# Optimization experiments

Measured on AMD Instinct MI355X. Metric: run time of the kernel, lower is better.

## Reference

```python
import jax, jax.numpy as jnp
import numpy as np

DIM = 768
NUM_HEADS = 12
HEAD_DIM = DIM // NUM_HEADS
SCALE = HEAD_DIM ** -0.5


def setup_inputs() -> dict:
    key = jax.random.key(0)
    ks = jax.random.split(key, 7)
    B, N = 4, 2048
    s = DIM ** -0.5
    return {
        "x": jax.random.normal(ks[0], (B, N, DIM), dtype=jnp.float32),
        "attn_bias": jax.random.normal(ks[1], (1, NUM_HEADS, N, N), dtype=jnp.float32),
        "Wq": jax.random.normal(ks[2], (DIM, DIM), dtype=jnp.float32) * s,
        "Wk": jax.random.normal(ks[3], (DIM, DIM), dtype=jnp.float32) * s,
        "Wv": jax.random.normal(ks[4], (DIM, DIM), dtype=jnp.float32) * s,
        "Wp": jax.random.normal(ks[5], (DIM, DIM), dtype=jnp.float32) * s,
        "bp": jax.random.normal(ks[6], (DIM,), dtype=jnp.float32) * 0.02,
    }


def reference(x, attn_bias, Wq, Wk, Wv, Wp, bp):
    B, N, C = x.shape
    # Linear layers use y = x @ W.T (torch convention); split heads: [B,H,N,D]
    def heads(y):
        return y.reshape(B, N, NUM_HEADS, HEAD_DIM).transpose(0, 2, 1, 3)
    q = heads(x @ Wq.T)
    k = heads(x @ Wk.T)
    v = heads(x @ Wv.T)
    attn = jnp.einsum("bhnd,bhmd->bhnm", q, k) * SCALE + attn_bias
    attn = jax.nn.softmax(attn, axis=-1)
    out = jnp.einsum("bhnm,bhmd->bhnd", attn, v)
    out = out.transpose(0, 2, 1, 3).reshape(B, N, C)
    return out @ Wp.T + bp
```

## Files before the change

kernel.cpp:

```cpp
#include <hip/hip_runtime.h>
#include <hip/hip_bf16.h>

#define NTOK 2048
#define NHEADS 12
#define HDIM 64
#define DIM 768
#define BATCH 4
#define SC2_ 0.18033688011112042f

typedef __attribute__((ext_vector_type(8))) short short8;
typedef __attribute__((ext_vector_type(4))) float f32x4;
typedef __attribute__((ext_vector_type(16))) float f32x16;

__device__ __forceinline__ short f2bf(float f) {
  union { float f; unsigned u; } v; v.f = f;
  unsigned r = v.u + 0x7fffu + ((v.u >> 16) & 1u);
  return (short)(r >> 16);
}

__device__ __forceinline__ f32x4 mfma_bf16(short8 a, short8 b, f32x4 c) {
  return __builtin_amdgcn_mfma_f32_16x16x32_bf16(a, b, c, 0, 0, 0);
}

__device__ __forceinline__ f32x16 mfma32(short8 a, short8 b, f32x16 c) {
  return __builtin_amdgcn_mfma_f32_32x32x16_bf16(a, b, c, 0, 0, 0);
}

__device__ __forceinline__ void gload_lds16(const void* g, void* l) {
  __builtin_amdgcn_global_load_lds((const __attribute__((address_space(1))) void*)g,
                                   (__attribute__((address_space(3))) void*)l, 16, 0, 0);
}

__device__ __forceinline__ float exp2_hw(float x) {
  float r; asm("v_exp_f32 %0, %1" : "=v"(r) : "v"(x)); return r;
}

__device__ __forceinline__ unsigned cvt_pk_bf16(float lo, float hi) {
  unsigned r; asm("v_cvt_pk_bf16_f32 %0, %1, %2" : "=v"(r) : "v"(lo), "v"(hi)); return r;
}

__global__ void cvt_x(const float* __restrict__ src, short* __restrict__ dst) {
  int i = blockIdx.x * 256 + threadIdx.x;
  float4 v = ((const float4*)src)[i];
  short4 o; o.x = f2bf(v.x); o.y = f2bf(v.y); o.z = f2bf(v.z); o.w = f2bf(v.w);
  ((short4*)dst)[i] = o;
}

__global__ void cvt_w(const float* __restrict__ w0, const float* __restrict__ w1,
                      const float* __restrict__ w2, const float* __restrict__ w3,
                      short* __restrict__ d0, short* __restrict__ d1,
                      short* __restrict__ d2, short* __restrict__ d3) {
  int i = blockIdx.x * 256 + threadIdx.x;
  const float* s = blockIdx.y == 0 ? w0 : blockIdx.y == 1 ? w1 : blockIdx.y == 2 ? w2 : w3;
  short* d = blockIdx.y == 0 ? d0 : blockIdx.y == 1 ? d1 : blockIdx.y == 2 ? d2 : d3;
  float4 v = ((const float4*)s)[i];
  short4 o; o.x = f2bf(v.x); o.y = f2bf(v.y); o.z = f2bf(v.z); o.w = f2bf(v.w);
  ((short4*)d)[i] = o;
}

__device__ __forceinline__ void gemm_mainloop(const short* __restrict__ A,
                                              const short* __restrict__ B,
                                              int mbase, int nbase,
                                              short* As, short* Bs,
                                              f32x4 (&acc)[4][4], int lane, int w) {
  int lr = lane & 15, lg = lane >> 4;
  int wr = w >> 1, wc = w & 1;
  for (int kb = 0; kb < DIM; kb += 64) {
    if (kb) __syncthreads();
#pragma unroll
    for (int c = 0; c < 4; ++c) {
      int row = w * 32 + c * 8 + (lane >> 3);
      int sch = (lane & 7) ^ (row & 7);
      gload_lds16(A + (size_t)(mbase + row) * DIM + kb + sch * 8, (char*)As + w * 4096 + c * 1024);
      gload_lds16(B + (size_t)(nbase + row) * DIM + kb + sch * 8, (char*)Bs + w * 4096 + c * 1024);
    }
    __syncthreads();
#pragma unroll
    for (int ks = 0; ks < 2; ++ks) {
      short8 af[4], bf[4];
#pragma unroll
      for (int i = 0; i < 4; ++i) {
        int row = wr * 64 + i * 16 + lr;
        int ch = (ks * 4 + lg) ^ (row & 7);
        af[i] = *(const short8*)(As + row * 64 + ch * 8);
      }
#pragma unroll
      for (int j = 0; j < 4; ++j) {
        int row = wc * 64 + j * 16 + lr;
        int ch = (ks * 4 + lg) ^ (row & 7);
        bf[j] = *(const short8*)(Bs + row * 64 + ch * 8);
      }
#pragma unroll
      for (int i = 0; i < 4; ++i)
#pragma unroll
        for (int j = 0; j < 4; ++j)
          acc[i][j] = mfma_bf16(af[i], bf[j], acc[i][j]);
    }
  }
}

__global__ __launch_bounds__(256, 2) void gemm_qkv(const short* __restrict__ xb,
    const short* __restrict__ wq, const short* __restrict__ wk, const short* __restrict__ wv,
    short* __restrict__ Qh, short* __restrict__ Kh, short* __restrict__ Vt) {
  __shared__ __align__(16) short As[128 * 64];
  __shared__ __align__(16) short Bs[128 * 64];
  int nt = blockIdx.x, mt = blockIdx.y, z = blockIdx.z;
  const short* B = z == 0 ? wq : (z == 1 ? wk : wv);
  int tid = threadIdx.x, lane = tid & 63, w = tid >> 6;
  f32x4 acc[4][4] = {};
  gemm_mainloop(xb, B, mt * 128, nt * 128, As, Bs, acc, lane, w);
  int lr = lane & 15, lg = lane >> 4, wr = w >> 1, wc = w & 1;
  if (z < 2) {
    short* dst = z == 0 ? Qh : Kh;
#pragma unroll
    for (int i = 0; i < 4; ++i)
#pragma unroll
      for (int j = 0; j < 4; ++j) {
        int m = mt * 128 + wr * 64 + i * 16 + lg * 4;
        int n = nt * 128 + wc * 64 + j * 16 + lr;
        int bb = m >> 11, nn = m & 2047, hh = n >> 6, d = n & 63;
        size_t base = (((size_t)bb * NHEADS + hh) * NTOK + nn) * HDIM + d;
#pragma unroll
        for (int r = 0; r < 4; ++r)
          dst[base + (size_t)r * HDIM] = f2bf(acc[i][j][r]);
      }
  } else {
#pragma unroll
    for (int i = 0; i < 4; ++i)
#pragma unroll
      for (int j = 0; j < 4; ++j) {
        int m = mt * 128 + wr * 64 + i * 16 + lg * 4;
        int n = nt * 128 + wc * 64 + j * 16 + lr;
        int bb = m >> 11, nn = m & 2047, hh = n >> 6, d = n & 63;
        short4 pk;
        pk.x = f2bf(acc[i][j][0]); pk.y = f2bf(acc[i][j][1]);
        pk.z = f2bf(acc[i][j][2]); pk.w = f2bf(acc[i][j][3]);
        *(short4*)(Vt + (((size_t)bb * NHEADS + hh) * HDIM + d) * NTOK + nn) = pk;
      }
  }
}

__global__ __launch_bounds__(256, 3) void attn_fused(const short* __restrict__ Qh,
    const short* __restrict__ Kh, const short* __restrict__ Vt,
    const float* __restrict__ bias, short* __restrict__ Ob) {
  __shared__ __align__(16) short Ks[2][64 * 64];
  __shared__ __align__(16) short Vs[2][64 * 64];
  int d0 = blockIdx.x;
  int wg = (d0 & 7) * 96 + (d0 >> 3);
  int b = wg & 3, qb = (wg >> 2) & 15, h = wg >> 6;
  int tid = threadIdx.x, lane = tid & 63, w = tid >> 6;
  int ql = lane & 31, hi = lane >> 5, sx = ql & 7;

  const short* Q = Qh + ((size_t)b * NHEADS + h) * NTOK * HDIM;
  const short* K = Kh + ((size_t)b * NHEADS + h) * NTOK * HDIM;
  const short* V = Vt + ((size_t)b * NHEADS + h) * HDIM * NTOK;
  int qrow = qb * 128 + w * 32 + ql;
  const float* Bb = bias + ((size_t)h * NTOK + qrow) * NTOK;

  short8 qf[4];
#pragma unroll
  for (int i = 0; i < 4; ++i)
    qf[i] = *(const short8*)(Q + (size_t)qrow * HDIM + i * 16 + hi * 8);

  float psum = 0.f;
  f32x16 oacc[2] = {};

  auto stage = [&](int buf, int kv) {
#pragma unroll
    for (int c = 0; c < 2; ++c) {
      int row = w * 16 + c * 8 + (lane >> 3);
      int sch = (lane & 7) ^ (lane >> 3);
      gload_lds16(K + (size_t)(kv + row) * HDIM + sch * 8, (char*)Ks[buf] + w * 2048 + c * 1024);
      gload_lds16(V + (size_t)row * NTOK + kv + sch * 8, (char*)Vs[buf] + w * 2048 + c * 1024);
    }
  };

  stage(0, 0);
  __syncthreads();

  auto body = [&](int t, int cur) {
    int kv = t * 64;

    f32x16 sacc[2];
#pragma unroll
    for (int kb = 0; kb < 2; ++kb)
#pragma unroll
      for (int g = 0; g < 4; ++g) {
        f32x4 bb = *(const f32x4*)(Bb + kv + kb * 32 + g * 8 + hi * 4);
#pragma unroll
        for (int r = 0; r < 4; ++r)
          sacc[kb][g * 4 + r] = fmaf(bb[r], 8.f, -128.f);
      }

    if (t < NTOK / 64 - 1) stage(cur ^ 1, kv + 64);

    __builtin_amdgcn_s_setprio(1);
#pragma unroll
    for (int kb = 0; kb < 2; ++kb)
#pragma unroll
      for (int i = 0; i < 4; ++i) {
        short8 kf = *(const short8*)(Ks[cur] + (kb * 32 + ql) * 64 + (((i * 2 + hi) ^ sx) * 8));
        sacc[kb] = mfma32(kf, qf[i], sacc[kb]);
      }
    __builtin_amdgcn_s_setprio(0);

#pragma unroll
    for (int kb = 0; kb < 2; ++kb) {
      float p[16];
#pragma unroll
      for (int rg = 0; rg < 16; ++rg) p[rg] = exp2_hw(sacc[kb][rg] * SC2_);
      float ts = 0.f;
#pragma unroll
      for (int g = 0; g < 4; ++g)
        ts += (p[g * 4] + p[g * 4 + 1]) + (p[g * 4 + 2] + p[g * 4 + 3]);
      psum += ts;
      unsigned Wd[4][2];
#pragma unroll
      for (int g = 0; g < 4; ++g)
#pragma unroll
        for (int tt = 0; tt < 2; ++tt)
          Wd[g][tt] = cvt_pk_bf16(p[g * 4 + tt * 2], p[g * 4 + tt * 2 + 1]);

#pragma unroll
      for (int cc = 0; cc < 2; ++cc) {
        auto r0 = __builtin_amdgcn_permlane32_swap(Wd[cc * 2][0], Wd[cc * 2 + 1][0], false, false);
        auto r1 = __builtin_amdgcn_permlane32_swap(Wd[cc * 2][1], Wd[cc * 2 + 1][1], false, false);
        union { unsigned u[4]; short8 s; } pb;
        pb.u[0] = r0[0]; pb.u[1] = r1[0]; pb.u[2] = r0[1]; pb.u[3] = r1[1];
        __builtin_amdgcn_s_setprio(1);
#pragma unroll
        for (int db = 0; db < 2; ++db) {
          short8 vf = *(const short8*)(Vs[cur] + (db * 32 + ql) * 64 + (((kb * 4 + cc * 2 + hi) ^ sx) * 8));
          oacc[db] = mfma32(vf, pb.s, oacc[db]);
        }
        __builtin_amdgcn_s_setprio(0);
      }
    }

    __syncthreads();
  };

  for (int t = 0; t < NTOK / 64; t += 2) {
    body(t, 0);
    body(t + 1, 1);
  }

  float fs = psum + __shfl_xor(psum, 32);
  float inv = 1.f / fs;
  size_t obase = ((size_t)b * NTOK + qrow) * DIM + h * HDIM;
#pragma unroll
  for (int db = 0; db < 2; ++db)
#pragma unroll
    for (int g = 0; g < 4; ++g) {
      unsigned u0 = cvt_pk_bf16(oacc[db][g * 4] * inv, oacc[db][g * 4 + 1] * inv);
      unsigned u1 = cvt_pk_bf16(oacc[db][g * 4 + 2] * inv, oacc[db][g * 4 + 3] * inv);
      uint2 pk; pk.x = u0; pk.y = u1;
      *(uint2*)(Ob + obase + db * 32 + g * 8 + hi * 4) = pk;
    }
}

__global__ __launch_bounds__(256, 2) void gemm_proj(const short* __restrict__ Ob,
    const short* __restrict__ wp, const float* __restrict__ bp, float* __restrict__ out) {
  __shared__ __align__(16) short As[128 * 64];
  __shared__ __align__(16) short Bs[128 * 64];
  int nt = blockIdx.x, mt = blockIdx.y;
  int tid = threadIdx.x, lane = tid & 63, w = tid >> 6;
  f32x4 acc[4][4] = {};
  gemm_mainloop(Ob, wp, mt * 128, nt * 128, As, Bs, acc, lane, w);
  int lr = lane & 15, lg = lane >> 4, wr = w >> 1, wc = w & 1;
#pragma unroll
  for (int j = 0; j < 4; ++j) {
    int n = nt * 128 + wc * 64 + j * 16 + lr;
    float bpv = bp[n];
#pragma unroll
    for (int i = 0; i < 4; ++i) {
      int m = mt * 128 + wr * 64 + i * 16 + lg * 4;
#pragma unroll
      for (int r = 0; r < 4; ++r)
        out[(size_t)(m + r) * DIM + n] = acc[i][j][r] + bpv;
    }
  }
}

extern "C" void kernel_launch(void* const* d_in, const int* in_sizes, int n_in,
                              void* d_out, int out_size, void* d_ws, size_t ws_size,
                              hipStream_t stream) {
  const float* x    = (const float*)d_in[0];
  const float* bias = (const float*)d_in[1];
  const float* Wq   = (const float*)d_in[2];
  const float* Wk   = (const float*)d_in[3];
  const float* Wv   = (const float*)d_in[4];
  const float* Wp   = (const float*)d_in[5];
  const float* bp   = (const float*)d_in[6];
  float* out = (float*)d_out;

  char* ws = (char*)d_ws;
  short* xb  = (short*)(ws);
  short* wqb = (short*)(ws + 12582912);
  short* wkb = (short*)(ws + 13762560);
  short* wvb = (short*)(ws + 14942208);
  short* wpb = (short*)(ws + 16121856);
  short* Qh  = (short*)(ws + 17301504);
  short* Kh  = (short*)(ws + 29884416);
  short* Vt  = (short*)(ws + 42467328);
  short* Ob  = (short*)(ws + 55050240);

  cvt_x<<<6144, 256, 0, stream>>>(x, xb);
  cvt_w<<<dim3(576, 4), 256, 0, stream>>>(Wq, Wk, Wv, Wp, wqb, wkb, wvb, wpb);
  gemm_qkv<<<dim3(6, 64, 3), 256, 0, stream>>>(xb, wqb, wkb, wvb, Qh, Kh, Vt);
  attn_fused<<<768, 256, 0, stream>>>(Qh, Kh, Vt, bias, Ob);
  gemm_proj<<<dim3(6, 64), 256, 0, stream>>>(Ob, wpb, bp, out);
}
```

Before: 214.7 us.

## Prefetch attention bias one tile ahead and change LDS swizzle pattern

The attention bias for the next KV tile is now loaded into a second register buffer while the current tile is computed, so global bias loads overlap the MFMA work. The K/V stage is issued at the start of the body, and the LDS XOR swizzle now mixes in the full row index (including the warp and chunk bits) to reduce bank conflicts. The s_setprio hints are removed. Double-buffering the bias costs 32 extra VGPRs per thread, which could reduce occupancy under the 3-blocks launch bound or cause spills.

```diff
diff --git a/kernel.cpp b/kernel.cpp
--- a/kernel.cpp
+++ b/kernel.cpp
@@ -149,7 +149,7 @@
   int wg = (d0 & 7) * 96 + (d0 >> 3);
   int b = wg & 3, qb = (wg >> 2) & 15, h = wg >> 6;
   int tid = threadIdx.x, lane = tid & 63, w = tid >> 6;
-  int ql = lane & 31, hi = lane >> 5, sx = ql & 7;
+  int ql = lane & 31, hi = lane >> 5;
 
   const short* Q = Qh + ((size_t)b * NHEADS + h) * NTOK * HDIM;
   const short* K = Kh + ((size_t)b * NHEADS + h) * NTOK * HDIM;
@@ -168,41 +168,51 @@
   auto stage = [&](int buf, int kv) {
 #pragma unroll
     for (int c = 0; c < 2; ++c) {
+      int srow = (lane >> 3) ^ (w * 2 + c);
+      int sch = (lane & 7) ^ srow;
       int row = w * 16 + c * 8 + (lane >> 3);
-      int sch = (lane & 7) ^ (lane >> 3);
       gload_lds16(K + (size_t)(kv + row) * HDIM + sch * 8, (char*)Ks[buf] + w * 2048 + c * 1024);
       gload_lds16(V + (size_t)row * NTOK + kv + sch * 8, (char*)Vs[buf] + w * 2048 + c * 1024);
     }
   };
 
+  auto loadBias = [&](int kv, f32x4 (&bv)[8]) {
+#pragma unroll
+    for (int g = 0; g < 8; ++g)
+      bv[g] = *(const f32x4*)(Bb + kv + g * 8 + hi * 4);
+  };
+
+  f32x4 bvA[8], bvB[8];
+  loadBias(0, bvA);
   stage(0, 0);
   __syncthreads();
 
-  auto body = [&](int t, int cur) {
+  auto body = [&](int t, int cur, f32x4 (&bvc)[8], f32x4 (&bvn)[8]) {
     int kv = t * 64;
+    bool more = t < NTOK / 64 - 1;
+    if (more) {
+      stage(cur ^ 1, kv + 64);
+      loadBias(kv + 64, bvn);
+    }
 
     f32x16 sacc[2];
 #pragma unroll
     for (int kb = 0; kb < 2; ++kb)
 #pragma unroll
-      for (int g = 0; g < 4; ++g) {
-        f32x4 bb = *(const f32x4*)(Bb + kv + kb * 32 + g * 8 + hi * 4);
+      for (int g = 0; g < 4; ++g)
 #pragma unroll
         for (int r = 0; r < 4; ++r)
-          sacc[kb][g * 4 + r] = fmaf(bb[r], 8.f, -128.f);
-      }
-
-    if (t < NTOK / 64 - 1) stage(cur ^ 1, kv + 64);
-
-    __builtin_amdgcn_s_setprio(1);
+          sacc[kb][g * 4 + r] = fmaf(bvc[kb * 4 + g][r], 8.f, -128.f);
+
 #pragma unroll
     for (int kb = 0; kb < 2; ++kb)
 #pragma unroll
       for (int i = 0; i < 4; ++i) {
-        short8 kf = *(const short8*)(Ks[cur] + (kb * 32 + ql) * 64 + (((i * 2 + hi) ^ sx) * 8));
+        int row = kb * 32 + ql;
+        int srow = (ql & 7) ^ (kb * 4 + (ql >> 3));
+        short8 kf = *(const short8*)(Ks[cur] + row * 64 + (((i * 2 + hi) ^ srow) * 8));
         sacc[kb] = mfma32(kf, qf[i], sacc[kb]);
       }
-    __builtin_amdgcn_s_setprio(0);
 
 #pragma unroll
     for (int kb = 0; kb < 2; ++kb) {
@@ -227,13 +237,13 @@
         auto r1 = __builtin_amdgcn_permlane32_swap(Wd[cc * 2][1], Wd[cc * 2 + 1][1], false, false);
         union { unsigned u[4]; short8 s; } pb;
         pb.u[0] = r0[0]; pb.u[1] = r1[0]; pb.u[2] = r0[1]; pb.u[3] = r1[1];
-        __builtin_amdgcn_s_setprio(1);
 #pragma unroll
         for (int db = 0; db < 2; ++db) {
-          short8 vf = *(const short8*)(Vs[cur] + (db * 32 + ql) * 64 + (((kb * 4 + cc * 2 + hi) ^ sx) * 8));
+          int row = db * 32 + ql;
+          int srow = (ql & 7) ^ (db * 4 + (ql >> 3));
+          short8 vf = *(const short8*)(Vs[cur] + row * 64 + (((kb * 4 + cc * 2 + hi) ^ srow) * 8));
           oacc[db] = mfma32(vf, pb.s, oacc[db]);
         }
-        __builtin_amdgcn_s_setprio(0);
       }
     }
 
@@ -241,8 +251,8 @@
   };
 
   for (int t = 0; t < NTOK / 64; t += 2) {
-    body(t, 0);
-    body(t + 1, 1);
+    body(t, 0, bvA, bvB);
+    body(t + 1, 1, bvB, bvA);
   }
 
   float fs = psum + __shfl_xor(psum, 32);
```

Result: slower. 260.6 us (+21.4%).
